# Kernel tuning notes

Hardware: AMD Instinct MI355X
Metric: run time of the kernel (lower is better)

The kernel has to match this reference:

```python
import jax, jax.numpy as jnp
import numpy as np

B, N, C, DFF, NH, KNN = 4, 2048, 256, 1024, 4, 16


def _gelu(x):
    return jax.nn.gelu(x, approximate=False)  # torch nn.GELU default = exact erf


def _ln(x, g, b, eps=1e-5):
    m = jnp.mean(x, axis=-1, keepdims=True)
    v = jnp.mean((x - m) ** 2, axis=-1, keepdims=True)
    return (x - m) * jax.lax.rsqrt(v + eps) * g + b


def setup_inputs() -> dict:
    key = jax.random.key(0)
    ks = jax.random.split(key, 16)
    w = lambda k, shp: jax.random.normal(k, shp, jnp.float32) * 0.02
    return {
        "src1": jax.random.normal(ks[0], (B, C, N), jnp.float32),
        "src2": jax.random.normal(ks[1], (B, C, N), jnp.float32),
        "pos": jax.random.uniform(ks[2], (B, 3, N), jnp.float32),
        # input_proj Conv1d(C, C, 1)
        "Wp": w(ks[3], (C, C)), "bp": jnp.zeros((C,), jnp.float32),
        # rel_pos_encoder: Conv2d(3, C//4, 1) -> GELU -> Conv2d(C//4, 1, 1)
        "Wr1": w(ks[4], (C // 4, 3)), "br1": jnp.zeros((C // 4,), jnp.float32),
        "Wr2": w(ks[5], (1, C // 4)), "br2": jnp.zeros((1,), jnp.float32),
        # MultiheadAttention packed in-proj + out-proj
        "Wqkv": w(ks[6], (3 * C, C)), "bqkv": jnp.zeros((3 * C,), jnp.float32),
        "Wo": w(ks[7], (C, C)), "bo": jnp.zeros((C,), jnp.float32),
        # norms
        "g13": jnp.ones((C,), jnp.float32), "b13": jnp.zeros((C,), jnp.float32),
        "g12": jnp.ones((C,), jnp.float32), "b12": jnp.zeros((C,), jnp.float32),
        # FFN
        "W1": w(ks[8], (DFF, C)), "b1": jnp.zeros((DFF,), jnp.float32),
        "W2": w(ks[9], (C, DFF)), "b2": jnp.zeros((C,), jnp.float32),
    }


def reference(src1, src2, pos, Wp, bp, Wr1, br1, Wr2, br2, Wqkv, bqkv,
              Wo, bo, g13, b13, g12, b12, W1, b1, W2, b2):
    b, _, n = src1.shape
    c = Wp.shape[0]
    h = NH
    dh = c // h

    # input_proj (1x1 conv == matmul over channel dim); go to (b, n, c)
    s1 = jnp.einsum('oc,bcn->bno', Wp, src1) + bp
    s2 = jnp.einsum('oc,bcn->bno', Wp, src2) + bp

    # --- KNN + rel-pos bias ---
    p = pos.transpose(0, 2, 1)  # (b, n, 3)
    sq = jnp.sum(p * p, axis=-1)  # (b, n)
    dist = sq[:, :, None] + sq[:, None, :] - 2.0 * jnp.einsum('bnd,bmd->bnm', p, p)
    _, idx = jax.lax.top_k(-dist, KNN)  # (b, n, KNN) nearest (incl. self)
    knn_pos = jax.vmap(lambda pp, ii: pp[ii])(p, idx)  # (b, n, KNN, 3)
    rel = p[:, :, None, :] - knn_pos  # (b, n, KNN, 3)
    hid = _gelu(jnp.einsum('bnkd,od->bnko', rel, Wr1) + br1)
    bias_vals = (jnp.einsum('bnko,uo->bnku', hid, Wr2) + br2)[..., 0]  # (b, n, KNN)

    attn_bias = jnp.full((b, n, n), -jnp.inf, dtype=s1.dtype)
    bi = jnp.arange(b)[:, None, None]
    ri = jnp.arange(n)[None, :, None]
    attn_bias = attn_bias.at[bi, ri, idx].set(bias_vals)  # scatter along dim 2

    # --- pre-norm (norm13 shared for q and kv) ---
    x1 = _ln(s1, g13, b13)
    x2 = _ln(s2, g13, b13)

    # --- multihead attention with additive float mask ---
    Wq, Wk, Wv = jnp.split(Wqkv, 3, axis=0)
    bq, bk, bv = jnp.split(bqkv, 3)
    q = (x1 @ Wq.T + bq).reshape(b, n, h, dh)
    k = (x2 @ Wk.T + bk).reshape(b, n, h, dh)
    v = (x2 @ Wv.T + bv).reshape(b, n, h, dh)
    scores = jnp.einsum('bqhd,bkhd->bhqk', q, k) / jnp.sqrt(jnp.asarray(dh, s1.dtype))
    scores = scores + attn_bias[:, None, :, :]  # repeat_interleave(nhead) == head broadcast
    attn = jax.nn.softmax(scores, axis=-1)
    o = jnp.einsum('bhqk,bkhd->bqhd', attn, v).reshape(b, n, c) @ Wo.T + bo

    x1 = _ln(x1 + o, g12, b12)
    ff = _gelu(x1 @ W1.T + b1) @ W2.T + b2
    out = x1 + ff
    return out.transpose(0, 2, 1)  # (b, c, n)
```

## Files before the change

kernel.cpp:

```cpp
#include <hip/hip_runtime.h>
#include <hip/hip_bf16.h>
#include <math.h>

constexpr int kB = 4;
constexpr int kN = 2048;
constexpr int kC = 256;
constexpr int kDFF = 1024;
constexpr int kKNN = 16;
constexpr int kDH = 64;

typedef __attribute__((ext_vector_type(8))) short short8;
typedef __attribute__((ext_vector_type(4))) short short4v;
typedef __attribute__((ext_vector_type(4))) float float4v;

__device__ __forceinline__ float gelu_erf(float x) {
    return 0.5f * x * (1.0f + erff(x * 0.70710678118654752440f));
}

__device__ __forceinline__ short f2b(float f) {
    unsigned u = __float_as_uint(f);
    u = u + 0x7FFFu + ((u >> 16) & 1u);
    return (short)(u >> 16);
}

__device__ __forceinline__ float b2f(short h) {
    unsigned u = ((unsigned)(unsigned short)h) << 16;
    return __uint_as_float(u);
}

__global__ __launch_bounds__(256) void cvt_all(
    const float* __restrict__ Wqkv, const float* __restrict__ Wo,
    const float* __restrict__ W1, const float* __restrict__ W2,
    const float* __restrict__ Wp, short* __restrict__ dst)
{
    const int i = (blockIdx.x * 256 + threadIdx.x) * 8;
    if (i < 786432) {
        const float* src; int off;
        if (i < 196608)      { src = Wqkv; off = i; }
        else if (i < 262144) { src = Wo;   off = i - 196608; }
        else if (i < 524288) { src = W1;   off = i - 262144; }
        else                 { src = W2;   off = i - 524288; }
        short8 v;
        #pragma unroll
        for (int j = 0; j < 8; j++) v[j] = f2b(src[off + j]);
        *(short8*)&dst[i] = v;
    } else {
        const int off = i - 786432;
        short8 h, l;
        #pragma unroll
        for (int j = 0; j < 8; j++) {
            float v = Wp[off + j];
            short hh = f2b(v);
            h[j] = hh;
            l[j] = f2b(v - b2f(hh));
        }
        *(short8*)&dst[786432 + off] = h;
        *(short8*)&dst[851968 + off] = l;
    }
}

__global__ __launch_bounds__(256) void transpose_cvt(
    const float* __restrict__ src1, const float* __restrict__ src2,
    short* __restrict__ hiT, short* __restrict__ loT)
{
    __shared__ float tile[32][33];
    const int z = blockIdx.z;
    const float* in = (z < 4 ? src1 : src2) + (size_t)(z & 3) * kC * kN;
    const int n0 = blockIdx.x * 32;
    const int c0 = blockIdx.y * 32;
    const int tx = threadIdx.x;
    const int ty = threadIdx.y;
    #pragma unroll
    for (int i = 0; i < 32; i += 8)
        tile[ty + i][tx] = in[(size_t)(c0 + ty + i) * kN + (n0 + tx)];
    __syncthreads();
    #pragma unroll
    for (int i = 0; i < 32; i += 8) {
        float v = tile[tx][ty + i];
        short h = f2b(v);
        short l = f2b(v - b2f(h));
        size_t o = ((size_t)z * kN + (n0 + ty + i)) * kC + (c0 + tx);
        hiT[o] = h;
        loT[o] = l;
    }
}

__global__ __launch_bounds__(256) void proj_mfma(
    const short* __restrict__ Ahi, const short* __restrict__ Alo,
    const short* __restrict__ Whi, const short* __restrict__ Wlo,
    const float* __restrict__ bias, float* __restrict__ out)
{
    __shared__ __align__(16) short AsmH[64][40], AsmL[64][40];
    __shared__ __align__(16) short BsmH[64][40], BsmL[64][40];

    const int tid = threadIdx.x;
    const int n0 = blockIdx.x * 64;
    const size_t m0 = (size_t)blockIdx.y * 64;
    const int lane = tid & 63, wv = tid >> 6;
    const int lm = lane & 15, quad = lane >> 4;
    const int r = tid >> 2, q = tid & 3;

    float4v acc[4] = {};

    for (int k0 = 0; k0 < kC; k0 += 32) {
        *(short8*)&AsmH[r][q * 8] = *(const short8*)&Ahi[(m0 + r) * kC + k0 + q * 8];
        *(short8*)&AsmL[r][q * 8] = *(const short8*)&Alo[(m0 + r) * kC + k0 + q * 8];
        *(short8*)&BsmH[r][q * 8] = *(const short8*)&Whi[(size_t)(n0 + r) * kC + k0 + q * 8];
        *(short8*)&BsmL[r][q * 8] = *(const short8*)&Wlo[(size_t)(n0 + r) * kC + k0 + q * 8];
        __syncthreads();

        short8 ah = *(const short8*)&AsmH[wv * 16 + lm][quad * 8];
        short8 al = *(const short8*)&AsmL[wv * 16 + lm][quad * 8];
        #pragma unroll
        for (int j4 = 0; j4 < 4; j4++) {
            short8 bh = *(const short8*)&BsmH[j4 * 16 + lm][quad * 8];
            short8 bl = *(const short8*)&BsmL[j4 * 16 + lm][quad * 8];
            acc[j4] = __builtin_amdgcn_mfma_f32_16x16x32_bf16(al, bh, acc[j4], 0, 0, 0);
            acc[j4] = __builtin_amdgcn_mfma_f32_16x16x32_bf16(ah, bl, acc[j4], 0, 0, 0);
            acc[j4] = __builtin_amdgcn_mfma_f32_16x16x32_bf16(ah, bh, acc[j4], 0, 0, 0);
        }
        __syncthreads();
    }

    #pragma unroll
    for (int j4 = 0; j4 < 4; j4++) {
        const int n = n0 + j4 * 16 + lm;
        const float bn = bias[n];
        #pragma unroll
        for (int rg = 0; rg < 4; rg++) {
            const size_t m = m0 + wv * 16 + quad * 4 + rg;
            out[m * kC + n] = acc[j4][rg] + bn;
        }
    }
}

__global__ __launch_bounds__(256) void mfma_gemm_bf(
    const short* __restrict__ A, const short* __restrict__ W,
    const float* __restrict__ bias, const float* __restrict__ resid,
    float* __restrict__ out, short* __restrict__ outbf,
    int M, int Nout, int K, int epi)
{
    __shared__ __align__(16) short Asm[64][72];
    __shared__ __align__(16) short Bsm[64][72];

    const int tid = threadIdx.x;
    const int n0 = blockIdx.x * 64;
    const int m0 = blockIdx.y * 64;
    const int lane = tid & 63, wv = tid >> 6;
    const int lm = lane & 15, quad = lane >> 4;
    const int r = tid >> 2, q = tid & 3;

    float4v acc[4] = {};

    for (int k0 = 0; k0 < K; k0 += 64) {
        const short* ap = &A[(size_t)(m0 + r) * K + k0 + q * 16];
        *(short8*)&Asm[r][q * 16]     = *(const short8*)ap;
        *(short8*)&Asm[r][q * 16 + 8] = *(const short8*)(ap + 8);
        const short* wp = &W[(size_t)(n0 + r) * K + k0 + q * 16];
        *(short8*)&Bsm[r][q * 16]     = *(const short8*)wp;
        *(short8*)&Bsm[r][q * 16 + 8] = *(const short8*)(wp + 8);
        __syncthreads();

        short8 af0 = *(const short8*)&Asm[wv * 16 + lm][quad * 8];
        short8 af1 = *(const short8*)&Asm[wv * 16 + lm][32 + quad * 8];
        #pragma unroll
        for (int j4 = 0; j4 < 4; j4++) {
            short8 bf0 = *(const short8*)&Bsm[j4 * 16 + lm][quad * 8];
            short8 bf1 = *(const short8*)&Bsm[j4 * 16 + lm][32 + quad * 8];
            acc[j4] = __builtin_amdgcn_mfma_f32_16x16x32_bf16(af0, bf0, acc[j4], 0, 0, 0);
            acc[j4] = __builtin_amdgcn_mfma_f32_16x16x32_bf16(af1, bf1, acc[j4], 0, 0, 0);
        }
        __syncthreads();
    }

    #pragma unroll
    for (int j4 = 0; j4 < 4; j4++) {
        const int n = n0 + j4 * 16 + lm;
        const float bn = bias[n];
        #pragma unroll
        for (int rg = 0; rg < 4; rg++) {
            const int m = m0 + wv * 16 + quad * 4 + rg;
            float v = acc[j4][rg] + bn;
            if (resid) v += resid[(size_t)m * Nout + n];
            if (epi == 1) v = gelu_erf(v);
            if (out)   out[(size_t)m * Nout + n] = v;
            if (outbf) outbf[(size_t)m * Nout + n] = f2b(v);
        }
    }
}

__global__ __launch_bounds__(256) void qkv_gemm(
    const short* __restrict__ x1bf, const short* __restrict__ x2bf,
    const short* __restrict__ Wqkvbf, const float* __restrict__ bqkv,
    float* __restrict__ qb, float* __restrict__ kvb)
{
    __shared__ __align__(16) short Asm[64][72];
    __shared__ __align__(16) short Bsm[64][72];

    const int n0g = blockIdx.x * 64;
    const int m0 = blockIdx.y * 64;
    const short* A; float* out; int Nout; int ncol0;
    if (n0g < 256) { A = x1bf; out = qb;  Nout = 256; ncol0 = n0g; }
    else           { A = x2bf; out = kvb; Nout = 512; ncol0 = n0g - 256; }

    const int tid = threadIdx.x;
    const int lane = tid & 63, wv = tid >> 6;
    const int lm = lane & 15, quad = lane >> 4;
    const int r = tid >> 2, q = tid & 3;

    float4v acc[4] = {};

    for (int k0 = 0; k0 < kC; k0 += 64) {
        const short* ap = &A[(size_t)(m0 + r) * kC + k0 + q * 16];
        *(short8*)&Asm[r][q * 16]     = *(const short8*)ap;
        *(short8*)&Asm[r][q * 16 + 8] = *(const short8*)(ap + 8);
        const short* wp = &Wqkvbf[(size_t)(n0g + r) * kC + k0 + q * 16];
        *(short8*)&Bsm[r][q * 16]     = *(const short8*)wp;
        *(short8*)&Bsm[r][q * 16 + 8] = *(const short8*)(wp + 8);
        __syncthreads();

        short8 af0 = *(const short8*)&Asm[wv * 16 + lm][quad * 8];
        short8 af1 = *(const short8*)&Asm[wv * 16 + lm][32 + quad * 8];
        #pragma unroll
        for (int j4 = 0; j4 < 4; j4++) {
            short8 bf0 = *(const short8*)&Bsm[j4 * 16 + lm][quad * 8];
            short8 bf1 = *(const short8*)&Bsm[j4 * 16 + lm][32 + quad * 8];
            acc[j4] = __builtin_amdgcn_mfma_f32_16x16x32_bf16(af0, bf0, acc[j4], 0, 0, 0);
            acc[j4] = __builtin_amdgcn_mfma_f32_16x16x32_bf16(af1, bf1, acc[j4], 0, 0, 0);
        }
        __syncthreads();
    }

    #pragma unroll
    for (int j4 = 0; j4 < 4; j4++) {
        const int nc = ncol0 + j4 * 16 + lm;
        const float bn = bqkv[n0g + j4 * 16 + lm];
        #pragma unroll
        for (int rg = 0; rg < 4; rg++) {
            const int m = m0 + wv * 16 + quad * 4 + rg;
            out[(size_t)m * Nout + nc] = acc[j4][rg] + bn;
        }
    }
}

__global__ __launch_bounds__(256) void ffn2_gemm_tr(
    const short* __restrict__ A, const short* __restrict__ W,
    const float* __restrict__ bias, const float* __restrict__ resid,
    float* __restrict__ out)
{
    __shared__ __align__(16) short Asm[64][72];
    __shared__ __align__(16) short Bsm[64][72];
    __shared__ float T[64][65];

    constexpr int K = kDFF;
    constexpr int Nout = kC;
    const int tid = threadIdx.x;
    const int n0 = blockIdx.x * 64;
    const int m0 = blockIdx.y * 64;
    const int lane = tid & 63, wv = tid >> 6;
    const int lm = lane & 15, quad = lane >> 4;
    const int r = tid >> 2, q = tid & 3;

    float4v acc[4] = {};

    for (int k0 = 0; k0 < K; k0 += 64) {
        const short* ap = &A[(size_t)(m0 + r) * K + k0 + q * 16];
        *(short8*)&Asm[r][q * 16]     = *(const short8*)ap;
        *(short8*)&Asm[r][q * 16 + 8] = *(const short8*)(ap + 8);
        const short* wp = &W[(size_t)(n0 + r) * K + k0 + q * 16];
        *(short8*)&Bsm[r][q * 16]     = *(const short8*)wp;
        *(short8*)&Bsm[r][q * 16 + 8] = *(const short8*)(wp + 8);
        __syncthreads();

        short8 af0 = *(const short8*)&Asm[wv * 16 + lm][quad * 8];
        short8 af1 = *(const short8*)&Asm[wv * 16 + lm][32 + quad * 8];
        #pragma unroll
        for (int j4 = 0; j4 < 4; j4++) {
            short8 bf0 = *(const short8*)&Bsm[j4 * 16 + lm][quad * 8];
            short8 bf1 = *(const short8*)&Bsm[j4 * 16 + lm][32 + quad * 8];
            acc[j4] = __builtin_amdgcn_mfma_f32_16x16x32_bf16(af0, bf0, acc[j4], 0, 0, 0);
            acc[j4] = __builtin_amdgcn_mfma_f32_16x16x32_bf16(af1, bf1, acc[j4], 0, 0, 0);
        }
        __syncthreads();
    }

    #pragma unroll
    for (int j4 = 0; j4 < 4; j4++) {
        const int nloc = j4 * 16 + lm;
        const float bn = bias[n0 + nloc];
        #pragma unroll
        for (int rg = 0; rg < 4; rg++) {
            const int mloc = wv * 16 + quad * 4 + rg;
            float v = acc[j4][rg] + bn;
            v += resid[(size_t)(m0 + mloc) * Nout + (n0 + nloc)];
            T[nloc][mloc] = v;
        }
    }
    __syncthreads();

    const int bidx = m0 >> 11;
    const int nb = m0 & 2047;
    const int nloc = tid >> 2;
    const int l4 = tid & 3;
    float* orow = out + (size_t)bidx * kC * kN + (size_t)(n0 + nloc) * kN + nb;
    #pragma unroll
    for (int i = 0; i < 4; i++) {
        const int mloc = l4 * 4 + i * 16;
        float4v v4;
        v4[0] = T[nloc][mloc];     v4[1] = T[nloc][mloc + 1];
        v4[2] = T[nloc][mloc + 2]; v4[3] = T[nloc][mloc + 3];
        *(float4v*)&orow[mloc] = v4;
    }
}

__global__ __launch_bounds__(256) void ln_kernel(
    float* __restrict__ x, short* __restrict__ xbf,
    const float* __restrict__ g, const float* __restrict__ bb, int wlim)
{
    const int lane = threadIdx.x & 63;
    const size_t row = (size_t)blockIdx.x * 4 + (threadIdx.x >> 6);

    float4v v = *(const float4v*)&x[row * kC + lane * 4];
    float s = (v[0] + v[1]) + (v[2] + v[3]);
    #pragma unroll
    for (int off = 32; off; off >>= 1) s += __shfl_xor(s, off, 64);
    const float mean = s * (1.0f / kC);

    float d0 = v[0] - mean, d1 = v[1] - mean, d2 = v[2] - mean, d3 = v[3] - mean;
    float s2 = (d0 * d0 + d1 * d1) + (d2 * d2 + d3 * d3);
    #pragma unroll
    for (int off = 32; off; off >>= 1) s2 += __shfl_xor(s2, off, 64);
    const float var = s2 * (1.0f / kC);
    const float r = 1.0f / sqrtf(var + 1e-5f);

    const float4v g4 = *(const float4v*)&g[lane * 4];
    const float4v b4 = *(const float4v*)&bb[lane * 4];
    float4v o;
    o[0] = d0 * r * g4[0] + b4[0];
    o[1] = d1 * r * g4[1] + b4[1];
    o[2] = d2 * r * g4[2] + b4[2];
    o[3] = d3 * r * g4[3] + b4[3];

    if ((int)row < wlim) *(float4v*)&x[row * kC + lane * 4] = o;
    short4v ob;
    ob[0] = f2b(o[0]); ob[1] = f2b(o[1]); ob[2] = f2b(o[2]); ob[3] = f2b(o[3]);
    *(short4v*)&xbf[row * kC + lane * 4] = ob;
}

#define KNN_RESCAN(CH, BM, BI)                                        \
    do {                                                              \
        float nb_ = 1e30f; int ni_ = kN;                              \
        _Pragma("unroll")                                             \
        for (int c8_ = 0; c8_ < 8; c8_++) {                           \
            int c_ = (CH) * 8 + c8_;                                  \
            float dd_ = (mask & (1u << c_)) ? 1e30f : cd[c_];         \
            if (dd_ < nb_) { nb_ = dd_; ni_ = c_ * 64 + lane; }       \
        }                                                             \
        BM = nb_; BI = ni_;                                           \
    } while (0)

__global__ __launch_bounds__(512) void knn_kernel(
    const float* __restrict__ pos,
    const float* __restrict__ Wr1, const float* __restrict__ br1,
    const float* __restrict__ Wr2, const float* __restrict__ br2,
    int* __restrict__ idx_out, float* __restrict__ bias_out)
{
    __shared__ float px[kN], py[kN], pz[kN];
    __shared__ int selS[8][kKNN];

    const int b = blockIdx.y;
    const int t = threadIdx.x;
    const int lane = t & 63, wv = t >> 6;
    const int n = blockIdx.x * 8 + wv;

    const float* pb = pos + (size_t)b * 3 * kN;
    for (int m = t; m < kN; m += 512) {
        px[m] = pb[m]; py[m] = pb[kN + m]; pz[m] = pb[2 * kN + m];
    }
    __syncthreads();

    const float qx = px[n], qy = py[n], qz = pz[n];
    const float qsq = __fadd_rn(__fadd_rn(__fmul_rn(qx, qx), __fmul_rn(qy, qy)),
                                __fmul_rn(qz, qz));

    float cd[32];
    float bm0 = 1e30f, bm1 = 1e30f, bm2 = 1e30f, bm3 = 1e30f;
    int bi0 = kN, bi1 = kN, bi2 = kN, bi3 = kN;
    #pragma unroll
    for (int c8 = 0; c8 < 8; c8++) {
        {
            const int c = c8, m = c * 64 + lane;
            float ax = px[m], ay = py[m], az = pz[m];
            float asq = __fadd_rn(__fadd_rn(__fmul_rn(ax, ax), __fmul_rn(ay, ay)), __fmul_rn(az, az));
            float dot = __fadd_rn(__fadd_rn(__fmul_rn(qx, ax), __fmul_rn(qy, ay)), __fmul_rn(qz, az));
            float d = __fsub_rn(__fadd_rn(qsq, asq), __fmul_rn(2.0f, dot));
            cd[c] = d;
            if (d < bm0) { bm0 = d; bi0 = m; }
        }
        {
            const int c = c8 + 8, m = c * 64 + lane;
            float ax = px[m], ay = py[m], az = pz[m];
            float asq = __fadd_rn(__fadd_rn(__fmul_rn(ax, ax), __fmul_rn(ay, ay)), __fmul_rn(az, az));
            float dot = __fadd_rn(__fadd_rn(__fmul_rn(qx, ax), __fmul_rn(qy, ay)), __fmul_rn(qz, az));
            float d = __fsub_rn(__fadd_rn(qsq, asq), __fmul_rn(2.0f, dot));
            cd[c] = d;
            if (d < bm1) { bm1 = d; bi1 = m; }
        }
        {
            const int c = c8 + 16, m = c * 64 + lane;
            float ax = px[m], ay = py[m], az = pz[m];
            float asq = __fadd_rn(__fadd_rn(__fmul_rn(ax, ax), __fmul_rn(ay, ay)), __fmul_rn(az, az));
            float dot = __fadd_rn(__fadd_rn(__fmul_rn(qx, ax), __fmul_rn(qy, ay)), __fmul_rn(qz, az));
            float d = __fsub_rn(__fadd_rn(qsq, asq), __fmul_rn(2.0f, dot));
            cd[c] = d;
            if (d < bm2) { bm2 = d; bi2 = m; }
        }
        {
            const int c = c8 + 24, m = c * 64 + lane;
            float ax = px[m], ay = py[m], az = pz[m];
            float asq = __fadd_rn(__fadd_rn(__fmul_rn(ax, ax), __fmul_rn(ay, ay)), __fmul_rn(az, az));
            float dot = __fadd_rn(__fadd_rn(__fmul_rn(qx, ax), __fmul_rn(qy, ay)), __fmul_rn(qz, az));
            float d = __fsub_rn(__fadd_rn(qsq, asq), __fmul_rn(2.0f, dot));
            cd[c] = d;
            if (d < bm3) { bm3 = d; bi3 = m; }
        }
    }

    unsigned mask = 0;
    for (int r = 0; r < kKNN; r++) {
        float best = bm0; int bid = bi0;
        if (bm1 < best) { best = bm1; bid = bi1; }
        if (bm2 < best) { best = bm2; bid = bi2; }
        if (bm3 < best) { best = bm3; bid = bi3; }

        #pragma unroll
        for (int off = 1; off < 64; off <<= 1) {
            float od = __shfl_xor(best, off, 64);
            int   oi = __shfl_xor(bid, off, 64);
            if (od < best || (od == best && oi < bid)) { best = od; bid = oi; }
        }
        if (lane == 0) selS[wv][r] = bid;
        if ((bid & 63) == lane) mask |= 1u << (bid >> 6);

        if (r < kKNN - 1) {
            const int sch = __builtin_amdgcn_readfirstlane(bid >> 9);
            switch (sch) {
                case 0:  KNN_RESCAN(0, bm0, bi0); break;
                case 1:  KNN_RESCAN(1, bm1, bi1); break;
                case 2:  KNN_RESCAN(2, bm2, bi2); break;
                default: KNN_RESCAN(3, bm3, bi3); break;
            }
        }
    }

    const int k = lane >> 2;
    const int part = lane & 3;
    const int m = selS[wv][k];
    const float rx = qx - px[m], ry = qy - py[m], rz = qz - pz[m];
    float partial = 0.0f;
    #pragma unroll
    for (int jj = 0; jj < 16; jj++) {
        int o = part * 16 + jj;
        float h = rx * Wr1[o * 3 + 0] + ry * Wr1[o * 3 + 1] +
                  rz * Wr1[o * 3 + 2] + br1[o];
        partial += gelu_erf(h) * Wr2[o];
    }
    partial += __shfl_xor(partial, 1, 64);
    partial += __shfl_xor(partial, 2, 64);
    if (part == 0) {
        size_t o = ((size_t)b * kN + n) * kKNN + k;
        idx_out[o] = m;
        bias_out[o] = partial + br2[0];
    }
}

__global__ __launch_bounds__(256) void attn_kernel(
    const float* __restrict__ q, const float* __restrict__ kv,
    const int* __restrict__ idx, const float* __restrict__ bias,
    short* __restrict__ obf)
{
    const int n = blockIdx.x;
    const int b = blockIdx.y;
    const int t = threadIdx.x;
    const int h = t >> 6;
    const int d = t & 63;

    const size_t row = (size_t)b * kN + n;
    const float qv = q[row * kC + h * kDH + d];

    __shared__ int   sidx[kKNN];
    __shared__ float sb[kKNN];
    if (t < kKNN) { sidx[t] = idx[row * kKNN + t]; sb[t] = bias[row * kKNN + t]; }
    __syncthreads();

    float sc[kKNN];
    #pragma unroll
    for (int j = 0; j < kKNN; j++) {
        size_t kr = (size_t)b * kN + sidx[j];
        float p = qv * kv[kr * 512 + h * kDH + d];
        #pragma unroll
        for (int off = 32; off; off >>= 1) p += __shfl_xor(p, off, 64);
        sc[j] = p * 0.125f + sb[j];
    }
    float mx = sc[0];
    #pragma unroll
    for (int j = 1; j < kKNN; j++) mx = fmaxf(mx, sc[j]);
    float den = 0.0f;
    #pragma unroll
    for (int j = 0; j < kKNN; j++) { sc[j] = expf(sc[j] - mx); den += sc[j]; }
    const float inv = 1.0f / den;
    float o = 0.0f;
    #pragma unroll
    for (int j = 0; j < kKNN; j++) {
        size_t kr = (size_t)b * kN + sidx[j];
        o += sc[j] * inv * kv[kr * 512 + kC + h * kDH + d];
    }
    obf[row * kC + h * kDH + d] = f2b(o);
}

extern "C" void kernel_launch(void* const* d_in, const int* in_sizes, int n_in,
                              void* d_out, int out_size, void* d_ws, size_t ws_size,
                              hipStream_t stream)
{
    const float* src1 = (const float*)d_in[0];
    const float* src2 = (const float*)d_in[1];
    const float* pos  = (const float*)d_in[2];
    const float* Wp   = (const float*)d_in[3];
    const float* bp   = (const float*)d_in[4];
    const float* Wr1  = (const float*)d_in[5];
    const float* br1  = (const float*)d_in[6];
    const float* Wr2  = (const float*)d_in[7];
    const float* br2  = (const float*)d_in[8];
    const float* Wqkv = (const float*)d_in[9];
    const float* bqkv = (const float*)d_in[10];
    const float* Wo   = (const float*)d_in[11];
    const float* bo   = (const float*)d_in[12];
    const float* g13  = (const float*)d_in[13];
    const float* b13  = (const float*)d_in[14];
    const float* g12  = (const float*)d_in[15];
    const float* b12  = (const float*)d_in[16];
    const float* W1   = (const float*)d_in[17];
    const float* b1   = (const float*)d_in[18];
    const float* W2   = (const float*)d_in[19];
    const float* b2   = (const float*)d_in[20];
    float* out = (float*)d_out;

    const size_t S = (size_t)kB * kN * kC;
    float* ws = (float*)d_ws;
    float* x1  = ws;
    float* s2  = ws + S;
    float* qb  = ws + 2 * S;
    float* kvb = ws + 3 * S;
    float* yb  = ws + 2 * S;
    short* srcThi = (short*)(ws + 2 * S);
    short* srcTlo = (short*)(ws + 3 * S);
    short* x1bf = (short*)(ws + 5 * S);
    short* x2bf = (short*)(ws + 5 * S) + S;
    short* ybf  = (short*)(ws + 6 * S);
    short* obf  = (short*)(ws + 6 * S) + S;
    short* hbf  = (short*)(ws + 3 * S);
    int*   idxb  = (int*)(ws + 7 * S);
    float* biasb = ws + 7 * S + (size_t)kB * kN * kKNN;
    short* wbf    = (short*)(ws + 7 * S + 2 * (size_t)kB * kN * kKNN);
    short* Wqkvbf = wbf;
    short* Wobf   = wbf + 196608;
    short* W1bf   = wbf + 262144;
    short* W2bf   = wbf + 524288;
    short* Wphi   = wbf + 786432;
    short* Wplo   = wbf + 851968;

    const int M = kB * kN;

    cvt_all<<<416, 256, 0, stream>>>(Wqkv, Wo, W1, W2, Wp, wbf);

    transpose_cvt<<<dim3(kN / 32, kC / 32, 8), dim3(32, 8), 0, stream>>>(
        src1, src2, srcThi, srcTlo);
    proj_mfma<<<dim3(kC / 64, 2 * M / 64), 256, 0, stream>>>(
        srcThi, srcTlo, Wphi, Wplo, bp, x1);

    ln_kernel<<<2 * M / 4, 256, 0, stream>>>(x1, x1bf, g13, b13, M);

    knn_kernel<<<dim3(kN / 8, kB), 512, 0, stream>>>(pos, Wr1, br1, Wr2, br2, idxb, biasb);

    qkv_gemm<<<dim3(12, M / 64), 256, 0, stream>>>(x1bf, x2bf, Wqkvbf, bqkv, qb, kvb);

    attn_kernel<<<dim3(kN, kB), 256, 0, stream>>>(qb, kvb, idxb, biasb, obf);

    mfma_gemm_bf<<<dim3(kC / 64, M / 64), 256, 0, stream>>>(
        obf, Wobf, bo, x1, yb, nullptr, M, kC, kC, 0);
    ln_kernel<<<M / 4, 256, 0, stream>>>(yb, ybf, g12, b12, M);

    mfma_gemm_bf<<<dim3(kDFF / 64, M / 64), 256, 0, stream>>>(
        ybf, W1bf, b1, nullptr, nullptr, hbf, M, kDFF, kC, 1);
    ffn2_gemm_tr<<<dim3(kC / 64, M / 64), 256, 0, stream>>>(
        hbf, W2bf, b2, yb, out);
}
```

Measured before the change: 280.8 us.

## Extract two nearest neighbours per wave-reduction round in KNN top-k selection

```diff
diff --git a/kernel.cpp b/kernel.cpp
--- a/kernel.cpp
+++ b/kernel.cpp
@@ -347,16 +347,34 @@
     *(short4v*)&xbf[row * kC + lane * 4] = ob;
 }
 
-#define KNN_RESCAN(CH, BM, BI)                                        \
+#define LEXLT(da, ma, db, mb) ((da) < (db) || ((da) == (db) && (ma) < (mb)))
+
+#define INS2(d_, m_, D1, M1, D2, M2)                                   \
+    if (LEXLT(d_, m_, D1, M1)) { D2 = D1; M2 = M1; D1 = d_; M1 = m_; } \
+    else if (LEXLT(d_, m_, D2, M2)) { D2 = d_; M2 = m_; }
+
+#define MERGE2(x1d, x1m, x2d, x2m, y1d, y1m, y2d, y2m, z1d, z1m, z2d, z2m)   \
+    if (LEXLT(x1d, x1m, y1d, y1m)) {                                         \
+        z1d = x1d; z1m = x1m;                                                \
+        if (LEXLT(x2d, x2m, y1d, y1m)) { z2d = x2d; z2m = x2m; }             \
+        else                           { z2d = y1d; z2m = y1m; }             \
+    } else {                                                                 \
+        z1d = y1d; z1m = y1m;                                                \
+        if (LEXLT(y2d, y2m, x1d, x1m)) { z2d = y2d; z2m = y2m; }             \
+        else                           { z2d = x1d; z2m = x1m; }             \
+    }
+
+#define KNN_RESCAN2(CH, D1, M1, D2, M2)                               \
     do {                                                              \
-        float nb_ = 1e30f; int ni_ = kN;                              \
+        float n1d_ = 1e30f, n2d_ = 1e30f; int n1m_ = kN, n2m_ = kN + 1; \
         _Pragma("unroll")                                             \
         for (int c8_ = 0; c8_ < 8; c8_++) {                           \
             int c_ = (CH) * 8 + c8_;                                  \
+            int m_ = c_ * 64 + lane;                                  \
             float dd_ = (mask & (1u << c_)) ? 1e30f : cd[c_];         \
-            if (dd_ < nb_) { nb_ = dd_; ni_ = c_ * 64 + lane; }       \
+            INS2(dd_, m_, n1d_, n1m_, n2d_, n2m_);                    \
         }                                                             \
-        BM = nb_; BI = ni_;                                           \
+        D1 = n1d_; M1 = n1m_; D2 = n2d_; M2 = n2m_;                   \
     } while (0)
 
 __global__ __launch_bounds__(512) void knn_kernel(
@@ -384,8 +402,10 @@
                                 __fmul_rn(qz, qz));
 
     float cd[32];
-    float bm0 = 1e30f, bm1 = 1e30f, bm2 = 1e30f, bm3 = 1e30f;
-    int bi0 = kN, bi1 = kN, bi2 = kN, bi3 = kN;
+    float a1d0 = 1e30f, a2d0 = 1e30f, a1d1 = 1e30f, a2d1 = 1e30f;
+    float a1d2 = 1e30f, a2d2 = 1e30f, a1d3 = 1e30f, a2d3 = 1e30f;
+    int a1m0 = kN, a2m0 = kN + 1, a1m1 = kN, a2m1 = kN + 1;
+    int a1m2 = kN, a2m2 = kN + 1, a1m3 = kN, a2m3 = kN + 1;
     #pragma unroll
     for (int c8 = 0; c8 < 8; c8++) {
         {
@@ -395,7 +415,7 @@
             float dot = __fadd_rn(__fadd_rn(__fmul_rn(qx, ax), __fmul_rn(qy, ay)), __fmul_rn(qz, az));
             float d = __fsub_rn(__fadd_rn(qsq, asq), __fmul_rn(2.0f, dot));
             cd[c] = d;
-            if (d < bm0) { bm0 = d; bi0 = m; }
+            INS2(d, m, a1d0, a1m0, a2d0, a2m0);
         }
         {
             const int c = c8 + 8, m = c * 64 + lane;
@@ -404,7 +424,7 @@
             float dot = __fadd_rn(__fadd_rn(__fmul_rn(qx, ax), __fmul_rn(qy, ay)), __fmul_rn(qz, az));
             float d = __fsub_rn(__fadd_rn(qsq, asq), __fmul_rn(2.0f, dot));
             cd[c] = d;
-            if (d < bm1) { bm1 = d; bi1 = m; }
+            INS2(d, m, a1d1, a1m1, a2d1, a2m1);
         }
         {
             const int c = c8 + 16, m = c * 64 + lane;
@@ -413,7 +433,7 @@
             float dot = __fadd_rn(__fadd_rn(__fmul_rn(qx, ax), __fmul_rn(qy, ay)), __fmul_rn(qz, az));
             float d = __fsub_rn(__fadd_rn(qsq, asq), __fmul_rn(2.0f, dot));
             cd[c] = d;
-            if (d < bm2) { bm2 = d; bi2 = m; }
+            INS2(d, m, a1d2, a1m2, a2d2, a2m2);
         }
         {
             const int c = c8 + 24, m = c * 64 + lane;
@@ -422,33 +442,51 @@
             float dot = __fadd_rn(__fadd_rn(__fmul_rn(qx, ax), __fmul_rn(qy, ay)), __fmul_rn(qz, az));
             float d = __fsub_rn(__fadd_rn(qsq, asq), __fmul_rn(2.0f, dot));
             cd[c] = d;
-            if (d < bm3) { bm3 = d; bi3 = m; }
+            INS2(d, m, a1d3, a1m3, a2d3, a2m3);
         }
     }
 
     unsigned mask = 0;
-    for (int r = 0; r < kKNN; r++) {
-        float best = bm0; int bid = bi0;
-        if (bm1 < best) { best = bm1; bid = bi1; }
-        if (bm2 < best) { best = bm2; bid = bi2; }
-        if (bm3 < best) { best = bm3; bid = bi3; }
-
+    for (int r = 0; r < kKNN / 2; r++) {
+        float p1d, p2d, q1d, q2d, L1d, L2d;
+        int p1m, p2m, q1m, q2m, L1m, L2m;
+        MERGE2(a1d0, a1m0, a2d0, a2m0, a1d1, a1m1, a2d1, a2m1, p1d, p1m, p2d, p2m);
+        MERGE2(a1d2, a1m2, a2d2, a2m2, a1d3, a1m3, a2d3, a2m3, q1d, q1m, q2d, q2m);
+        MERGE2(p1d, p1m, p2d, p2m, q1d, q1m, q2d, q2m, L1d, L1m, L2d, L2m);
+
+        float g1d = L1d, g2d = L2d;
+        int g1m = L1m, g2m = L2m;
         #pragma unroll
         for (int off = 1; off < 64; off <<= 1) {
-            float od = __shfl_xor(best, off, 64);
-            int   oi = __shfl_xor(bid, off, 64);
-            if (od < best || (od == best && oi < bid)) { best = od; bid = oi; }
-        }
-        if (lane == 0) selS[wv][r] = bid;
-        if ((bid & 63) == lane) mask |= 1u << (bid >> 6);
-
-        if (r < kKNN - 1) {
-            const int sch = __builtin_amdgcn_readfirstlane(bid >> 9);
-            switch (sch) {
-                case 0:  KNN_RESCAN(0, bm0, bi0); break;
-                case 1:  KNN_RESCAN(1, bm1, bi1); break;
-                case 2:  KNN_RESCAN(2, bm2, bi2); break;
-                default: KNN_RESCAN(3, bm3, bi3); break;
+            float o1d = __shfl_xor(g1d, off, 64);
+            float o2d = __shfl_xor(g2d, off, 64);
+            int   o1m = __shfl_xor(g1m, off, 64);
+            int   o2m = __shfl_xor(g2m, off, 64);
+            float t1d, t2d; int t1m, t2m;
+            MERGE2(g1d, g1m, g2d, g2m, o1d, o1m, o2d, o2m, t1d, t1m, t2d, t2m);
+            g1d = t1d; g1m = t1m; g2d = t2d; g2m = t2m;
+        }
+
+        if (lane == 0) { selS[wv][2 * r] = g1m; selS[wv][2 * r + 1] = g2m; }
+        if ((g1m & 63) == lane) mask |= 1u << (g1m >> 6);
+        if ((g2m & 63) == lane) mask |= 1u << (g2m >> 6);
+
+        if (r < kKNN / 2 - 1) {
+            const int sch1 = __builtin_amdgcn_readfirstlane(g1m >> 9);
+            const int sch2 = __builtin_amdgcn_readfirstlane(g2m >> 9);
+            switch (sch1) {
+                case 0:  KNN_RESCAN2(0, a1d0, a1m0, a2d0, a2m0); break;
+                case 1:  KNN_RESCAN2(1, a1d1, a1m1, a2d1, a2m1); break;
+                case 2:  KNN_RESCAN2(2, a1d2, a1m2, a2d2, a2m2); break;
+                default: KNN_RESCAN2(3, a1d3, a1m3, a2d3, a2m3); break;
+            }
+            if (sch2 != sch1) {
+                switch (sch2) {
+                    case 0:  KNN_RESCAN2(0, a1d0, a1m0, a2d0, a2m0); break;
+                    case 1:  KNN_RESCAN2(1, a1d1, a1m1, a2d1, a2m1); break;
+                    case 2:  KNN_RESCAN2(2, a1d2, a1m2, a2d2, a2m2); break;
+                    default: KNN_RESCAN2(3, a1d3, a1m3, a2d3, a2m3); break;
+                }
             }
         }
     }
```

New measurement: 312.9 us. 11.4% more time.
